# Optimization experiments

Hardware: AMD Instinct MI355X
Metric: run time of the kernel (lower is better)

The kernel has to match this reference:

```python
import jax, jax.numpy as jnp
import numpy as np

N_NODES = 100000
N_EDGES = 3200000
K_HOPS = 10
ALPHA = 0.1


def setup_inputs() -> dict:
    key = jax.random.key(0)
    ks = jax.random.split(key, 7)
    x = jax.random.normal(ks[0], (N_NODES, 500), dtype=jnp.float32)
    edge_index = jax.random.randint(ks[1], (2, N_EDGES), 0, N_NODES, dtype=jnp.int32)
    W1 = jax.random.normal(ks[2], (500, 64), dtype=jnp.float32) * 0.05
    b1 = jax.random.normal(ks[3], (64,), dtype=jnp.float32) * 0.05
    W2 = jax.random.normal(ks[4], (64, 64), dtype=jnp.float32) * 0.1
    b2 = jax.random.normal(ks[5], (64,), dtype=jnp.float32) * 0.05
    # PPR init: temp[k] = alpha*(1-alpha)^k, temp[K] = (1-alpha)^K
    temp = ALPHA * (1.0 - ALPHA) ** np.arange(K_HOPS + 1)
    temp[-1] = (1.0 - ALPHA) ** K_HOPS
    temp = jnp.asarray(temp, dtype=jnp.float32)
    return {"x": x, "edge_index": edge_index, "W1": W1, "b1": b1,
            "W2": W2, "b2": b2, "temp": temp}


def reference(x, edge_index, W1, b1, W2, b2, temp):
    n = x.shape[0]
    # MLP (dropout is identity in eval mode)
    h = jax.nn.relu(x @ W1 + b1)
    h = h @ W2 + b2  # [N, C]

    # gcn_norm with self-loops (edge_weight=None -> all ones)
    loops = jnp.arange(n, dtype=edge_index.dtype)
    row = jnp.concatenate([edge_index[0], loops])  # source (x_j)
    col = jnp.concatenate([edge_index[1], loops])  # target (aggregate)
    w = jnp.ones(row.shape[0], dtype=h.dtype)
    deg = jax.ops.segment_sum(w, col, num_segments=n)
    dinv = jnp.where(deg > 0, jax.lax.rsqrt(deg), 0.0)
    norm = dinv[row] * w * dinv[col]  # [E+N]

    # GPR propagation: hidden = sum_k temp[k] * A_hat^k h
    hidden = h * temp[0]
    cur = h
    for k in range(K_HOPS):
        cur = jax.ops.segment_sum(norm[:, None] * cur[row], col, num_segments=n)
        hidden = hidden + temp[k + 1] * cur

    return jax.nn.log_softmax(hidden, axis=1)
```

## Files before the change

kernel.cpp:

```cpp
#include <hip/hip_runtime.h>
#include <hip/hip_bf16.h>
#include <math.h>

#define FEAT_IN 500
#define HID 64
#define NPB 128
#define MAXB 1024

typedef unsigned int uint;
typedef unsigned short ushort;
typedef __attribute__((ext_vector_type(8))) short bf16x8;
typedef __attribute__((ext_vector_type(4))) float f32x4;

__device__ inline ushort f2bf(float f) {
    uint u = __float_as_uint(f);
    uint r = (u + 0x7fff + ((u >> 16) & 1)) >> 16;
    return (ushort)r;
}

__device__ inline uint pk2(float a, float b) {
    uint ua = __float_as_uint(a), ub = __float_as_uint(b);
    ua = ua + 0x7fff + ((ua >> 16) & 1);
    ub = ub + 0x7fff + ((ub >> 16) & 1);
    return (ua >> 16) | (ub & 0xffff0000u);
}

__device__ inline void bf8_unpack(const uint4 v, float f[8]) {
    f[0] = __uint_as_float(v.x << 16);
    f[1] = __uint_as_float(v.x & 0xffff0000u);
    f[2] = __uint_as_float(v.y << 16);
    f[3] = __uint_as_float(v.y & 0xffff0000u);
    f[4] = __uint_as_float(v.z << 16);
    f[5] = __uint_as_float(v.z & 0xffff0000u);
    f[6] = __uint_as_float(v.w << 16);
    f[7] = __uint_as_float(v.w & 0xffff0000u);
}

__global__ __launch_bounds__(256) void bcnt_kernel(const int* __restrict__ col,
                                                   int* __restrict__ bcnt, int E, int nbkt) {
    __shared__ int cnt[MAXB];
    int tid = threadIdx.x;
    for (int j = tid; j < nbkt; j += 256) cnt[j] = 0;
    __syncthreads();
    int stride = gridDim.x * 256;
    for (int e = blockIdx.x * 256 + tid; e < E; e += stride) {
        atomicAdd(&cnt[col[e] >> 7], 1);
    }
    __syncthreads();
    for (int j = tid; j < nbkt; j += 256) {
        int v = cnt[j];
        if (v) atomicAdd(&bcnt[j], v);
    }
}

__global__ void bscan_kernel(const int* __restrict__ bcnt, int* __restrict__ boff,
                             int* __restrict__ bcur, int* __restrict__ ptr,
                             int nbkt, int n, int E) {
    int lane = threadIdx.x;
    int run = 0;
    for (int base = 0; base < nbkt; base += 64) {
        int i = base + lane;
        int v = (i < nbkt) ? bcnt[i] : 0;
        int sc = v;
#pragma unroll
        for (int d = 1; d < 64; d <<= 1) {
            int t = __shfl_up(sc, d);
            if (lane >= d) sc += t;
        }
        if (i < nbkt) {
            int ex = run + sc - v;
            boff[i] = ex;
            bcur[i] = ex;
        }
        run += __shfl(sc, 63);
    }
    if (lane == 0) {
        boff[nbkt] = E;
        ptr[n] = E;
    }
}

__global__ __launch_bounds__(1024) void bscat_kernel(const int* __restrict__ row,
                                                     const int* __restrict__ col,
                                                     int* __restrict__ bcur,
                                                     uint* __restrict__ csr_tmp,
                                                     int E, int nbkt) {
    __shared__ int cnt[MAXB];
    __shared__ int pos[MAXB];
    int tid = threadIdx.x;
    int chunk = (E + gridDim.x - 1) / gridDim.x;
    int c0 = blockIdx.x * chunk;
    int c1 = min(E, c0 + chunk);
    for (int j = tid; j < nbkt; j += 1024) cnt[j] = 0;
    __syncthreads();
    for (int e = c0 + tid; e < c1; e += 1024) atomicAdd(&cnt[col[e] >> 7], 1);
    __syncthreads();
    for (int j = tid; j < nbkt; j += 1024) {
        int v = cnt[j];
        pos[j] = v ? atomicAdd(&bcur[j], v) : 0;
    }
    __syncthreads();
    for (int e = c0 + tid; e < c1; e += 1024) {
        int c = col[e];
        int j = c >> 7;
        int r = atomicAdd(&pos[j], 1);
        csr_tmp[r] = ((uint)row[e] << 7) | (uint)(c & (NPB - 1));
    }
}

__global__ __launch_bounds__(256) void bsort_kernel(const uint* __restrict__ csr_tmp,
                                                    const int* __restrict__ boff,
                                                    int* __restrict__ ptr,
                                                    float* __restrict__ dinv,
                                                    int* __restrict__ csr_src,
                                                    int n) {
    __shared__ int degl[NPB];
    __shared__ int offl[NPB];
    int b = blockIdx.x;
    int tid = threadIdx.x;
    int t0 = boff[b], t1 = boff[b + 1];
    if (tid < NPB) degl[tid] = 0;
    __syncthreads();
    for (int p = t0 + tid; p < t1; p += 256) {
        uint pk = csr_tmp[p];
        atomicAdd(&degl[pk & (NPB - 1)], 1);
    }
    __syncthreads();
    if (tid < 64) {
        int v0 = degl[tid];
        int s0 = v0;
#pragma unroll
        for (int d = 1; d < 64; d <<= 1) {
            int t = __shfl_up(s0, d);
            if (tid >= d) s0 += t;
        }
        int tot0 = __shfl(s0, 63);
        int v1 = degl[64 + tid];
        int s1 = v1;
#pragma unroll
        for (int d = 1; d < 64; d <<= 1) {
            int t = __shfl_up(s1, d);
            if (tid >= d) s1 += t;
        }
        offl[tid] = s0 - v0;
        offl[64 + tid] = tot0 + s1 - v1;
    }
    __syncthreads();
    if (tid < NPB) {
        int node = b * NPB + tid;
        if (node < n) {
            ptr[node] = t0 + offl[tid];
            dinv[node] = rsqrtf((float)(degl[tid] + 1));
        }
    }
    __syncthreads();
    for (int p = t0 + tid; p < t1; p += 256) {
        uint pk = csr_tmp[p];
        int l = pk & (NPB - 1);
        int r = t0 + atomicAdd(&offl[l], 1);
        csr_src[r] = (int)(pk >> 7);
    }
}

__global__ void swz_kernel(const float* __restrict__ W1, const float* __restrict__ W2,
                           ushort* __restrict__ w1s, ushort* __restrict__ w2s) {
    int idx = blockIdx.x * blockDim.x + threadIdx.x;
    if (idx < 32768) {
        int j = idx & 7;
        int l = (idx >> 3) & 63;
        int t = (idx >> 9) & 3;
        int c = idx >> 11;
        int k = c * 32 + (l >> 4) * 8 + j;
        int nn = t * 16 + (l & 15);
        float v = (k < FEAT_IN) ? W1[(size_t)k * HID + nn] : 0.0f;
        w1s[idx] = f2bf(v);
    } else if (idx < 32768 + 4096) {
        int r = idx - 32768;
        int j = r & 7;
        int l = (r >> 3) & 63;
        int t = (r >> 9) & 3;
        int c = r >> 11;
        int k = c * 32 + (l >> 4) * 8 + j;
        int nn = t * 16 + (l & 15);
        w2s[r] = f2bf(W2[(size_t)k * HID + nn]);
    }
}

__global__ __launch_bounds__(256) void mlp_kernel(const float* __restrict__ x,
                                                  const ushort* __restrict__ w1s,
                                                  const float* __restrict__ b1,
                                                  const ushort* __restrict__ w2s,
                                                  const float* __restrict__ b2,
                                                  const float* __restrict__ temp,
                                                  const float* __restrict__ dinv,
                                                  ushort* __restrict__ A,
                                                  float* __restrict__ out, int n) {
    __shared__ float pacc[2][2][16][65];
    __shared__ ushort hls[2][16 * 72];
    const int tid = threadIdx.x;
    const int lane = tid & 63;
    const int wv = tid >> 6;
    const int tl = wv >> 1;
    const int kh = wv & 1;
    const int g = lane >> 4;
    const int c15 = lane & 15;
    const int nmt = (n + 15) / 16;
    int mt = blockIdx.x * 2 + tl;
    bool mtok = (mt < nmt);
    float t0 = temp[0];

    f32x4 acc[4] = {{0.f, 0.f, 0.f, 0.f}, {0.f, 0.f, 0.f, 0.f},
                    {0.f, 0.f, 0.f, 0.f}, {0.f, 0.f, 0.f, 0.f}};
    int row = mt * 16 + c15;
    bool rok = mtok && (row < n);
    const float* xr = x + (size_t)row * FEAT_IN;

    if (mtok) {
        const int cbeg = kh * 8;
        const int cend = kh ? 15 : 8;
        float4 L0 = {0.f, 0.f, 0.f, 0.f}, H0 = L0, L1 = L0, H1 = L0;
        if (rok) {
            L0 = *(const float4*)(xr + cbeg * 32 + g * 8);
            H0 = *(const float4*)(xr + cbeg * 32 + g * 8 + 4);
            L1 = *(const float4*)(xr + (cbeg + 1) * 32 + g * 8);
            H1 = *(const float4*)(xr + (cbeg + 1) * 32 + g * 8 + 4);
        }
        for (int c = cbeg; c < cend; c++) {
            float4 Ln = {0.f, 0.f, 0.f, 0.f}, Hn = Ln;
            int cn = c + 2;
            if (rok && cn < cend) {
                Ln = *(const float4*)(xr + cn * 32 + g * 8);
                Hn = *(const float4*)(xr + cn * 32 + g * 8 + 4);
            }
            uint4 au;
            au.x = pk2(L0.x, L0.y);
            au.y = pk2(L0.z, L0.w);
            au.z = pk2(H0.x, H0.y);
            au.w = pk2(H0.z, H0.w);
            bf16x8 a = *(bf16x8*)&au;
            const ushort* wp = w1s + ((size_t)c * 4) * 512 + lane * 8;
#pragma unroll
            for (int t = 0; t < 4; t++) {
                bf16x8 b = *(const bf16x8*)(wp + t * 512);
                acc[t] = __builtin_amdgcn_mfma_f32_16x16x32_bf16(a, b, acc[t], 0, 0, 0);
            }
            L0 = L1; H0 = H1; L1 = Ln; H1 = Hn;
        }
        if (kh) {
            float v[8];
#pragma unroll
            for (int j = 0; j < 8; j++) {
                int k = 480 + g * 8 + j;
                v[j] = (rok && k < FEAT_IN) ? xr[k] : 0.0f;
            }
            uint4 au;
            au.x = pk2(v[0], v[1]);
            au.y = pk2(v[2], v[3]);
            au.z = pk2(v[4], v[5]);
            au.w = pk2(v[6], v[7]);
            bf16x8 a = *(bf16x8*)&au;
            const ushort* wp = w1s + (size_t)15 * 4 * 512 + lane * 8;
#pragma unroll
            for (int t = 0; t < 4; t++) {
                bf16x8 b = *(const bf16x8*)(wp + t * 512);
                acc[t] = __builtin_amdgcn_mfma_f32_16x16x32_bf16(a, b, acc[t], 0, 0, 0);
            }
        }
#pragma unroll
        for (int t = 0; t < 4; t++) {
#pragma unroll
            for (int r = 0; r < 4; r++) {
                pacc[tl][kh][g * 4 + r][t * 16 + c15] = acc[t][r];
            }
        }
    }
    __syncthreads();

    if (mtok) {
        int rrow = lane & 15;
        int cg = lane >> 4;
        int colbase = kh * 32 + cg * 8;
#pragma unroll
        for (int cc = 0; cc < 8; cc++) {
            int colc = colbase + cc;
            float h = pacc[tl][0][rrow][colc] + pacc[tl][1][rrow][colc] + b1[colc];
            hls[tl][rrow * 72 + colc] = f2bf(fmaxf(h, 0.0f));
        }
    }
    __syncthreads();
    if (!mtok) return;

    f32x4 acc2[2] = {{0.f, 0.f, 0.f, 0.f}, {0.f, 0.f, 0.f, 0.f}};
#pragma unroll
    for (int c2 = 0; c2 < 2; c2++) {
        bf16x8 a2 = *(const bf16x8*)(hls[tl] + c15 * 72 + c2 * 32 + g * 8);
#pragma unroll
        for (int tt = 0; tt < 2; tt++) {
            int t = kh * 2 + tt;
            bf16x8 b = *(const bf16x8*)(w2s + ((size_t)(c2 * 4 + t)) * 512 + lane * 8);
            acc2[tt] = __builtin_amdgcn_mfma_f32_16x16x32_bf16(a2, b, acc2[tt], 0, 0, 0);
        }
    }

#pragma unroll
    for (int tt = 0; tt < 2; tt++) {
        int t = kh * 2 + tt;
        float b2v = b2[t * 16 + c15];
#pragma unroll
        for (int r = 0; r < 4; r++) {
            int orow = mt * 16 + g * 4 + r;
            if (orow < n) {
                float dres = acc2[tt][r] + b2v;
                size_t o = (size_t)orow * HID + t * 16 + c15;
                A[o] = f2bf(dinv[orow] * dres);
                out[o] = t0 * dres;
            }
        }
    }
}

__global__ __launch_bounds__(256) void hopf_kernel(const int* __restrict__ ptr,
                                                   const int* __restrict__ csr_src,
                                                   const float* __restrict__ dinv,
                                                   const ushort* __restrict__ cur,
                                                   ushort* __restrict__ nxt,
                                                   float* __restrict__ out,
                                                   const float* __restrict__ temp,
                                                   const ushort* __restrict__ Sbase,
                                                   int tidx, int Kf, int defer, int n) {
    int i = (blockIdx.x * blockDim.x + threadIdx.x) >> 6;
    int lane = threadIdx.x & 63;
    if (i >= n) return;
    const int g = lane >> 3;
    const int q = lane & 7;
    const size_t nf = (size_t)n * HID;

    int s = ptr[i];
    int e = ptr[i + 1];
    const uint* curu = (const uint*)cur;

    float acc[8] = {0.f, 0.f, 0.f, 0.f, 0.f, 0.f, 0.f, 0.f};
    float accB[8] = {0.f, 0.f, 0.f, 0.f, 0.f, 0.f, 0.f, 0.f};

    int rounds = (e - s + 31) >> 5;
    int p = s + g;
    int j0 = csr_src[(p      < e) ? p      : 0];
    int j1 = csr_src[(p + 8  < e) ? p + 8  : 0];
    int j2 = csr_src[(p + 16 < e) ? p + 16 : 0];
    int j3 = csr_src[(p + 24 < e) ? p + 24 : 0];

    for (int r = 0; r < rounds; r++) {
        int pn = p + 32;
        int k0 = csr_src[(pn      < e) ? pn      : 0];
        int k1 = csr_src[(pn + 8  < e) ? pn + 8  : 0];
        int k2 = csr_src[(pn + 16 < e) ? pn + 16 : 0];
        int k3 = csr_src[(pn + 24 < e) ? pn + 24 : 0];
        uint4 v0 = *(const uint4*)(curu + (size_t)j0 * 32 + q * 4);
        uint4 v1 = *(const uint4*)(curu + (size_t)j1 * 32 + q * 4);
        uint4 v2 = *(const uint4*)(curu + (size_t)j2 * 32 + q * 4);
        uint4 v3 = *(const uint4*)(curu + (size_t)j3 * 32 + q * 4);
        float w0 = (p      < e) ? 1.0f : 0.0f;
        float w1 = (p + 8  < e) ? 1.0f : 0.0f;
        float w2 = (p + 16 < e) ? 1.0f : 0.0f;
        float w3 = (p + 24 < e) ? 1.0f : 0.0f;
        float f[8];
        bf8_unpack(v0, f);
#pragma unroll
        for (int t = 0; t < 8; t++) acc[t] += w0 * f[t];
        bf8_unpack(v1, f);
#pragma unroll
        for (int t = 0; t < 8; t++) accB[t] += w1 * f[t];
        bf8_unpack(v2, f);
#pragma unroll
        for (int t = 0; t < 8; t++) acc[t] += w2 * f[t];
        bf8_unpack(v3, f);
#pragma unroll
        for (int t = 0; t < 8; t++) accB[t] += w3 * f[t];
        p = pn;
        j0 = k0; j1 = k1; j2 = k2; j3 = k3;
    }
#pragma unroll
    for (int t = 0; t < 8; t++) acc[t] += accB[t];

#pragma unroll
    for (int m = 8; m <= 32; m <<= 1) {
#pragma unroll
        for (int t = 0; t < 8; t++) acc[t] += __shfl_xor(acc[t], m);
    }

    uint4 sv = *(const uint4*)(curu + (size_t)i * 32 + q * 4);
    float sf[8];
    bf8_unpack(sv, sf);
#pragma unroll
    for (int t = 0; t < 8; t++) acc[t] += sf[t];

    if (lane < 8) {
        float d = dinv[i];
        float dd = d * d;
        float tk = temp[tidx] * d;
        if (tidx < Kf) {
            uint4 pk;
            pk.x = (uint)f2bf(dd * acc[0]) | ((uint)f2bf(dd * acc[1]) << 16);
            pk.y = (uint)f2bf(dd * acc[2]) | ((uint)f2bf(dd * acc[3]) << 16);
            pk.z = (uint)f2bf(dd * acc[4]) | ((uint)f2bf(dd * acc[5]) << 16);
            pk.w = (uint)f2bf(dd * acc[6]) | ((uint)f2bf(dd * acc[7]) << 16);
            *(uint4*)((uint*)nxt + (size_t)i * 32 + q * 4) = pk;

            if (!defer) {
                float* op = out + (size_t)i * HID + q * 8;
                float4 o0 = *(const float4*)(op);
                float4 o1 = *(const float4*)(op + 4);
                o0.x += tk * acc[0]; o0.y += tk * acc[1]; o0.z += tk * acc[2]; o0.w += tk * acc[3];
                o1.x += tk * acc[4]; o1.y += tk * acc[5]; o1.z += tk * acc[6]; o1.w += tk * acc[7];
                *(float4*)(op) = o0;
                *(float4*)(op + 4) = o1;
            }
        } else {
            float* op = out + (size_t)i * HID + q * 8;
            float4 o0 = *(const float4*)(op);
            float4 o1 = *(const float4*)(op + 4);
            if (defer) {
                float rd = 1.0f / d;
                for (int k = 1; k < Kf; k++) {
                    const uint* sp = (const uint*)(Sbase + (size_t)k * nf) + (size_t)i * 32 + q * 4;
                    uint4 v = *(const uint4*)sp;
                    float f[8];
                    bf8_unpack(v, f);
                    float c = temp[k] * rd;
                    o0.x += c * f[0]; o0.y += c * f[1]; o0.z += c * f[2]; o0.w += c * f[3];
                    o1.x += c * f[4]; o1.y += c * f[5]; o1.z += c * f[6]; o1.w += c * f[7];
                }
            }
            o0.x += tk * acc[0]; o0.y += tk * acc[1]; o0.z += tk * acc[2]; o0.w += tk * acc[3];
            o1.x += tk * acc[4]; o1.y += tk * acc[5]; o1.z += tk * acc[6]; o1.w += tk * acc[7];

            float m = fmaxf(fmaxf(fmaxf(o0.x, o0.y), fmaxf(o0.z, o0.w)),
                            fmaxf(fmaxf(o1.x, o1.y), fmaxf(o1.z, o1.w)));
#pragma unroll
            for (int dm = 1; dm <= 4; dm <<= 1) m = fmaxf(m, __shfl_xor(m, dm));
            float ex = expf(o0.x - m) + expf(o0.y - m) + expf(o0.z - m) + expf(o0.w - m)
                     + expf(o1.x - m) + expf(o1.y - m) + expf(o1.z - m) + expf(o1.w - m);
#pragma unroll
            for (int dm = 1; dm <= 4; dm <<= 1) ex += __shfl_xor(ex, dm);
            float L = m + logf(ex);
            o0.x -= L; o0.y -= L; o0.z -= L; o0.w -= L;
            o1.x -= L; o1.y -= L; o1.z -= L; o1.w -= L;
            *(float4*)(op) = o0;
            *(float4*)(op + 4) = o1;
        }
    }
}

__global__ __launch_bounds__(256) void lsm_kernel(float* __restrict__ out, int n) {
    int i = (blockIdx.x * blockDim.x + threadIdx.x) >> 6;
    int lane = threadIdx.x & 63;
    if (i >= n) return;
    size_t o = (size_t)i * HID + lane;
    float v = out[o];
    float m = v;
#pragma unroll
    for (int d = 32; d >= 1; d >>= 1) m = fmaxf(m, __shfl_xor(m, d));
    float ex = expf(v - m);
#pragma unroll
    for (int d = 32; d >= 1; d >>= 1) ex += __shfl_xor(ex, d);
    out[o] = v - m - logf(ex);
}

extern "C" void kernel_launch(void* const* d_in, const int* in_sizes, int n_in,
                              void* d_out, int out_size, void* d_ws, size_t ws_size,
                              hipStream_t stream) {
    const float* x    = (const float*)d_in[0];
    const int*   ei   = (const int*)d_in[1];
    const float* W1   = (const float*)d_in[2];
    const float* b1   = (const float*)d_in[3];
    const float* W2   = (const float*)d_in[4];
    const float* b2   = (const float*)d_in[5];
    const float* temp = (const float*)d_in[6];

    int n = in_sizes[0] / FEAT_IN;
    int E = in_sizes[1] / 2;
    int K = in_sizes[6] - 1;
    const int* row = ei;
    const int* col = ei + E;
    int nbkt = (n + NPB - 1) >> 7;

    char* ws = (char*)d_ws;
    size_t off = 0;
    auto alloc = [&](size_t bytes) -> void* {
        void* p = (void*)(ws + off);
        off += (bytes + 255) & ~(size_t)255;
        return p;
    };
    float* dinv    = (float*)alloc((size_t)n * sizeof(float));
    int*   ptr     = (int*)alloc((size_t)(n + 1) * sizeof(int));
    int*   bcnt    = (int*)alloc((size_t)MAXB * sizeof(int));
    int*   boff    = (int*)alloc((size_t)(MAXB + 1) * sizeof(int));
    int*   bcur    = (int*)alloc((size_t)MAXB * sizeof(int));
    uint*  csr_tmp = (uint*)alloc((size_t)E * sizeof(uint));
    int*   csr_src = (int*)alloc((size_t)E * sizeof(int));
    ushort* w1s    = (ushort*)alloc(32768 * sizeof(ushort));
    ushort* w2s    = (ushort*)alloc(4096 * sizeof(ushort));

    size_t nf = (size_t)n * HID;
    size_t rem = (off <= ws_size) ? (ws_size - off) : 0;
    int defer = 0;
    ushort *A, *B, *S = nullptr;
    if (K > 1 && rem >= (size_t)K * nf * sizeof(ushort) + 1024) {
        defer = 1;
        S = (ushort*)alloc((size_t)K * nf * sizeof(ushort));
        A = S;
        B = S;
    } else {
        A = (ushort*)alloc(nf * sizeof(ushort));
        B = (ushort*)alloc(nf * sizeof(ushort));
        S = A;
    }

    float* out = (float*)d_out;

    hipMemsetAsync(bcnt, 0, (size_t)nbkt * sizeof(int), stream);

    bcnt_kernel<<<256, 256, 0, stream>>>(col, bcnt, E, nbkt);
    bscan_kernel<<<1, 64, 0, stream>>>(bcnt, boff, bcur, ptr, nbkt, n, E);
    bscat_kernel<<<256, 1024, 0, stream>>>(row, col, bcur, csr_tmp, E, nbkt);
    bsort_kernel<<<nbkt, 256, 0, stream>>>(csr_tmp, boff, ptr, dinv, csr_src, n);
    swz_kernel<<<(32768 + 4096 + 255) / 256, 256, 0, stream>>>(W1, W2, w1s, w2s);

    int nmt = (n + 15) / 16;
    int mlp_blocks = (nmt + 1) / 2;
    mlp_kernel<<<mlp_blocks, 256, 0, stream>>>(x, w1s, b1, w2s, b2, temp, dinv, A, out, n);

    int hop_blocks = (n + 3) / 4;
    if (defer) {
        for (int k = 0; k < K; k++) {
            const ushort* cur = S + (size_t)k * nf;
            ushort* nxt = (k + 1 < K) ? (S + (size_t)(k + 1) * nf) : S;
            hopf_kernel<<<hop_blocks, 256, 0, stream>>>(ptr, csr_src, dinv, cur, nxt, out,
                                                        temp, S, k + 1, K, 1, n);
        }
    } else {
        ushort* cur = A;
        ushort* nxt = B;
        for (int k = 0; k < K; k++) {
            hopf_kernel<<<hop_blocks, 256, 0, stream>>>(ptr, csr_src, dinv, cur, nxt, out,
                                                        temp, S, k + 1, K, 0, n);
            ushort* t = cur; cur = nxt; nxt = t;
        }
    }
    if (K == 0) {
        lsm_kernel<<<hop_blocks, 256, 0, stream>>>(out, n);
    }
}
```

Before: 1.025 ms.

## Split bf16 hop features into two column-half planes with per-half gather kernel

The bf16 propagated features are stored as two planes of 32 columns each instead of 64-wide rows. The intermediate hops run a new kernel that gathers only one half-plane per block, so blocks alternate between the halves. This shrinks the working set each gather touches, aiming for better L2/MALL hit rates on the random neighbour reads. In exchange it doubles the number of blocks and the csr_src index reads, and uses 64-byte gathers instead of 128-byte ones.

Measured after the change: 1.324 ms. 29.1% more time.

```diff
diff --git a/kernel.cpp b/kernel.cpp
--- a/kernel.cpp
+++ b/kernel.cpp
@@ -208,6 +208,7 @@
     int mt = blockIdx.x * 2 + tl;
     bool mtok = (mt < nmt);
     float t0 = temp[0];
+    const size_t half = (size_t)n * 32;
 
     f32x4 acc[4] = {{0.f, 0.f, 0.f, 0.f}, {0.f, 0.f, 0.f, 0.f},
                     {0.f, 0.f, 0.f, 0.f}, {0.f, 0.f, 0.f, 0.f}};
@@ -311,11 +312,84 @@
             int orow = mt * 16 + g * 4 + r;
             if (orow < n) {
                 float dres = acc2[tt][r] + b2v;
-                size_t o = (size_t)orow * HID + t * 16 + c15;
-                A[o] = f2bf(dinv[orow] * dres);
-                out[o] = t0 * dres;
-            }
-        }
+                A[(size_t)(t >> 1) * half + (size_t)orow * 32 + (t & 1) * 16 + c15] =
+                    f2bf(dinv[orow] * dres);
+                out[(size_t)orow * HID + t * 16 + c15] = t0 * dres;
+            }
+        }
+    }
+}
+
+__global__ __launch_bounds__(256) void hopt2_kernel(const int* __restrict__ ptr,
+                                                    const int* __restrict__ csr_src,
+                                                    const float* __restrict__ dinv,
+                                                    const ushort* __restrict__ cur,
+                                                    ushort* __restrict__ nxt, int n) {
+    int b = blockIdx.x;
+    int tile = b & 1;
+    int grp = b >> 1;
+    int wv = threadIdx.x >> 6;
+    int lane = threadIdx.x & 63;
+    int i = grp * 4 + wv;
+    if (i >= n) return;
+    const int slot = lane >> 2;
+    const int q = lane & 3;
+    const size_t half_u = (size_t)n * 16;
+    const uint* curt = (const uint*)cur + (size_t)tile * half_u + q * 4;
+
+    int s = ptr[i];
+    int e = ptr[i + 1];
+
+    float acc[8] = {0.f, 0.f, 0.f, 0.f, 0.f, 0.f, 0.f, 0.f};
+    float accB[8] = {0.f, 0.f, 0.f, 0.f, 0.f, 0.f, 0.f, 0.f};
+
+    int rounds = (e - s + 31) >> 5;
+    int p = s + slot;
+    int j0 = csr_src[(p      < e) ? p      : 0];
+    int j1 = csr_src[(p + 16 < e) ? p + 16 : 0];
+
+    for (int r = 0; r < rounds; r++) {
+        int pn = p + 32;
+        int k0 = csr_src[(pn      < e) ? pn      : 0];
+        int k1 = csr_src[(pn + 16 < e) ? pn + 16 : 0];
+        uint4 v0 = *(const uint4*)(curt + (size_t)j0 * 16);
+        uint4 v1 = *(const uint4*)(curt + (size_t)j1 * 16);
+        float w0 = (p      < e) ? 1.0f : 0.0f;
+        float w1 = (p + 16 < e) ? 1.0f : 0.0f;
+        float f[8];
+        bf8_unpack(v0, f);
+#pragma unroll
+        for (int t = 0; t < 8; t++) acc[t] += w0 * f[t];
+        bf8_unpack(v1, f);
+#pragma unroll
+        for (int t = 0; t < 8; t++) accB[t] += w1 * f[t];
+        p = pn;
+        j0 = k0; j1 = k1;
+    }
+#pragma unroll
+    for (int t = 0; t < 8; t++) acc[t] += accB[t];
+
+#pragma unroll
+    for (int m = 4; m <= 32; m <<= 1) {
+#pragma unroll
+        for (int t = 0; t < 8; t++) acc[t] += __shfl_xor(acc[t], m);
+    }
+
+    uint4 sv = *(const uint4*)(curt + (size_t)i * 16);
+    float sf[8];
+    bf8_unpack(sv, sf);
+#pragma unroll
+    for (int t = 0; t < 8; t++) acc[t] += sf[t];
+
+    if (lane < 4) {
+        float d = dinv[i];
+        float dd = d * d;
+        uint4 pk;
+        pk.x = (uint)f2bf(dd * acc[0]) | ((uint)f2bf(dd * acc[1]) << 16);
+        pk.y = (uint)f2bf(dd * acc[2]) | ((uint)f2bf(dd * acc[3]) << 16);
+        pk.z = (uint)f2bf(dd * acc[4]) | ((uint)f2bf(dd * acc[5]) << 16);
+        pk.w = (uint)f2bf(dd * acc[6]) | ((uint)f2bf(dd * acc[7]) << 16);
+        *(uint4*)((uint*)nxt + (size_t)tile * half_u + (size_t)i * 16 + lane * 4) = pk;
     }
 }
 
@@ -334,10 +408,12 @@
     const int g = lane >> 3;
     const int q = lane & 7;
     const size_t nf = (size_t)n * HID;
+    const size_t half_u = (size_t)n * 16;
+    const size_t qoff = (size_t)(q >> 2) * half_u + (q & 3) * 4;
+    const uint* curt = (const uint*)cur + qoff;
 
     int s = ptr[i];
     int e = ptr[i + 1];
-    const uint* curu = (const uint*)cur;
 
     float acc[8] = {0.f, 0.f, 0.f, 0.f, 0.f, 0.f, 0.f, 0.f};
     float accB[8] = {0.f, 0.f, 0.f, 0.f, 0.f, 0.f, 0.f, 0.f};
@@ -355,10 +431,10 @@
         int k1 = csr_src[(pn + 8  < e) ? pn + 8  : 0];
         int k2 = csr_src[(pn + 16 < e) ? pn + 16 : 0];
         int k3 = csr_src[(pn + 24 < e) ? pn + 24 : 0];
-        uint4 v0 = *(const uint4*)(curu + (size_t)j0 * 32 + q * 4);
-        uint4 v1 = *(const uint4*)(curu + (size_t)j1 * 32 + q * 4);
-        uint4 v2 = *(const uint4*)(curu + (size_t)j2 * 32 + q * 4);
-        uint4 v3 = *(const uint4*)(curu + (size_t)j3 * 32 + q * 4);
+        uint4 v0 = *(const uint4*)(curt + (size_t)j0 * 16);
+        uint4 v1 = *(const uint4*)(curt + (size_t)j1 * 16);
+        uint4 v2 = *(const uint4*)(curt + (size_t)j2 * 16);
+        uint4 v3 = *(const uint4*)(curt + (size_t)j3 * 16);
         float w0 = (p      < e) ? 1.0f : 0.0f;
         float w1 = (p + 8  < e) ? 1.0f : 0.0f;
         float w2 = (p + 16 < e) ? 1.0f : 0.0f;
@@ -388,7 +464,7 @@
         for (int t = 0; t < 8; t++) acc[t] += __shfl_xor(acc[t], m);
     }
 
-    uint4 sv = *(const uint4*)(curu + (size_t)i * 32 + q * 4);
+    uint4 sv = *(const uint4*)(curt + (size_t)i * 16);
     float sf[8];
     bf8_unpack(sv, sf);
 #pragma unroll
@@ -404,7 +480,7 @@
             pk.y = (uint)f2bf(dd * acc[2]) | ((uint)f2bf(dd * acc[3]) << 16);
             pk.z = (uint)f2bf(dd * acc[4]) | ((uint)f2bf(dd * acc[5]) << 16);
             pk.w = (uint)f2bf(dd * acc[6]) | ((uint)f2bf(dd * acc[7]) << 16);
-            *(uint4*)((uint*)nxt + (size_t)i * 32 + q * 4) = pk;
+            *(uint4*)((uint*)nxt + qoff + (size_t)i * 16) = pk;
 
             if (!defer) {
                 float* op = out + (size_t)i * HID + q * 8;
@@ -422,7 +498,7 @@
             if (defer) {
                 float rd = 1.0f / d;
                 for (int k = 1; k < Kf; k++) {
-                    const uint* sp = (const uint*)(Sbase + (size_t)k * nf) + (size_t)i * 32 + q * 4;
+                    const uint* sp = (const uint*)(Sbase + (size_t)k * nf) + qoff + (size_t)i * 16;
                     uint4 v = *(const uint4*)sp;
                     float f[8];
                     bf8_unpack(v, f);
@@ -530,24 +606,25 @@
     int mlp_blocks = (nmt + 1) / 2;
     mlp_kernel<<<mlp_blocks, 256, 0, stream>>>(x, w1s, b1, w2s, b2, temp, dinv, A, out, n);
 
-    int hop_blocks = (n + 3) / 4;
+    int ng = (n + 3) / 4;
     if (defer) {
-        for (int k = 0; k < K; k++) {
-            const ushort* cur = S + (size_t)k * nf;
-            ushort* nxt = (k + 1 < K) ? (S + (size_t)(k + 1) * nf) : S;
-            hopf_kernel<<<hop_blocks, 256, 0, stream>>>(ptr, csr_src, dinv, cur, nxt, out,
-                                                        temp, S, k + 1, K, 1, n);
-        }
+        for (int k = 0; k < K - 1; k++) {
+            hopt2_kernel<<<2 * ng, 256, 0, stream>>>(ptr, csr_src, dinv,
+                                                     S + (size_t)k * nf,
+                                                     S + (size_t)(k + 1) * nf, n);
+        }
+        hopf_kernel<<<ng, 256, 0, stream>>>(ptr, csr_src, dinv, S + (size_t)(K - 1) * nf,
+                                            S, out, temp, S, K, K, 1, n);
     } else {
         ushort* cur = A;
         ushort* nxt = B;
         for (int k = 0; k < K; k++) {
-            hopf_kernel<<<hop_blocks, 256, 0, stream>>>(ptr, csr_src, dinv, cur, nxt, out,
-                                                        temp, S, k + 1, K, 0, n);
+            hopf_kernel<<<ng, 256, 0, stream>>>(ptr, csr_src, dinv, cur, nxt, out,
+                                                temp, S, k + 1, K, 0, n);
             ushort* t = cur; cur = nxt; nxt = t;
         }
     }
     if (K == 0) {
-        lsm_kernel<<<hop_blocks, 256, 0, stream>>>(out, n);
-    }
-}
+        lsm_kernel<<<ng, 256, 0, stream>>>(out, n);
+    }
+}
```
